# Kernel tuning notes

Hardware: AMD Instinct MI355X
Metric: run time of the kernel (lower is better)

The kernel has to match this reference:

```python
import jax, jax.numpy as jnp
import numpy as np

BN_EPS = 1e-6


def _conv1x1(x, w, b):
    # x: (B, Cin, N, K), w: (Cout, Cin), b: (Cout,)
    return jnp.einsum('oc,bcnk->bonk', w, x) + b[None, :, None, None]


def _bn(x, gamma, beta, mean, var):
    # inference-mode BatchNorm2d over channel axis 1
    inv = gamma / jnp.sqrt(var + BN_EPS)
    return x * inv[None, :, None, None] + (beta - mean * inv)[None, :, None, None]


def setup_inputs() -> dict:
    key = jax.random.key(0)
    ks = jax.random.split(key, 12)
    B, N, K = 4, 16384, 16
    C_out = 32
    C_img = 2 * C_out - 10          # 54, so concat has 2*C_out = 64 channels
    C_in1 = 2 * C_out               # 64
    C_in2 = 2 * (C_out + 3)         # 70

    points = jax.random.normal(ks[0], (B, N, 3), jnp.float32)
    image_features = jax.random.normal(ks[1], (B, C_img, N, K), jnp.float32)
    dist = jax.random.uniform(ks[2], (B, N, K), jnp.float32)
    idx = jax.random.randint(ks[3], (B, N, K), 0, N, dtype=jnp.int32)

    w1 = jax.random.normal(ks[4], (C_out, C_in1), jnp.float32) / np.sqrt(C_in1).astype(np.float32)
    b1 = jnp.zeros((C_out,), jnp.float32)
    gamma1 = jnp.ones((C_out,), jnp.float32)
    beta1 = jnp.zeros((C_out,), jnp.float32)
    mean1 = 0.1 * jax.random.normal(ks[5], (C_out,), jnp.float32)
    var1 = 0.5 + jax.random.uniform(ks[6], (C_out,), jnp.float32)

    w2 = jax.random.normal(ks[7], (C_out, C_in2), jnp.float32) / np.sqrt(C_in2).astype(np.float32)
    b2 = jnp.zeros((C_out,), jnp.float32)
    gamma2 = jnp.ones((C_out,), jnp.float32)
    beta2 = jnp.zeros((C_out,), jnp.float32)
    mean2 = 0.1 * jax.random.normal(ks[8], (C_out,), jnp.float32)
    var2 = 0.5 + jax.random.uniform(ks[9], (C_out,), jnp.float32)

    return {
        'points': points, 'image_features': image_features, 'dist': dist, 'idx': idx,
        'w1': w1, 'b1': b1, 'gamma1': gamma1, 'beta1': beta1, 'mean1': mean1, 'var1': var1,
        'w2': w2, 'b2': b2, 'gamma2': gamma2, 'beta2': beta2, 'mean2': mean2, 'var2': var2,
    }


def reference(points, image_features, dist, idx,
              w1, b1, gamma1, beta1, mean1, var1,
              w2, b2, gamma2, beta2, mean2, var2):
    B, N, K = idx.shape
    pts = jnp.swapaxes(points, 1, 2)                       # (B, 3, N)
    ep = jnp.broadcast_to(pts[:, :, :, None], (B, 3, N, K))  # extended points
    # KNN gather: nb[b, c, n, k] = pts[b, c, idx[b, n, k]]
    nb = jax.vmap(lambda p, i: p[:, i])(pts, idx)          # (B, 3, N, K)

    concat = jnp.concatenate(
        [ep, nb, ep - nb, dist[:, None, :, :], image_features], axis=1)  # (B, 64, N, K)

    h = jax.nn.relu(_bn(_conv1x1(concat, w1, b1), gamma1, beta1, mean1, var1))  # (B, 32, N, K)
    feat = jnp.concatenate([h, ep], axis=1)                # (B, 35, N, K)

    pooled = jnp.concatenate(
        [jnp.max(feat, axis=-1, keepdims=True),
         jnp.mean(feat, axis=-1, keepdims=True)], axis=1)  # (B, 70, N, 1)

    out = jax.nn.relu(_bn(_conv1x1(pooled, w2, b2), gamma2, beta2, mean2, var2))  # (B, 32, N, 1)
    return out
```

## Files before the change

kernel.cpp:

```cpp
#include <hip/hip_runtime.h>
#include <hip/hip_bf16.h>
#include <cmath>

#define BN_EPS 1e-6f
typedef unsigned int u32;
typedef __attribute__((ext_vector_type(8))) short short8;
typedef __attribute__((ext_vector_type(4))) float f32x4;

constexpr int B_    = 4;
constexpr int N_    = 16384;
constexpr int K_    = 16;
constexpr int C_IMG = 54;
constexpr int C1    = 64;
constexpr int CO    = 32;
constexpr int C2    = 70;
constexpr int NT    = 16;
constexpr int POS   = 256;
constexpr int XSTR  = 34;
constexpr int PPAD  = 76;
constexpr int NK    = N_ * K_;
constexpr int CHUNK = 6;

__device__ inline u32 pkbf(float a, float b) {
    union { __hip_bfloat162 h; u32 u; } cv;
    cv.h = __float22bfloat162_rn(make_float2(a, b));
    return cv.u;
}

__global__ __launch_bounds__(256, 4) void pif_mfma_kernel(
    const float* __restrict__ points, const float* __restrict__ imgf,
    const float* __restrict__ dist,   const int*   __restrict__ idx,
    const float* __restrict__ w1, const float* __restrict__ b1,
    const float* __restrict__ g1, const float* __restrict__ be1,
    const float* __restrict__ m1, const float* __restrict__ v1,
    const float* __restrict__ w2, const float* __restrict__ b2,
    const float* __restrict__ g2, const float* __restrict__ be2,
    const float* __restrict__ m2, const float* __restrict__ v2,
    float* __restrict__ out)
{
    __shared__ u32   x_lds[POS * XSTR];
    __shared__ float pooled[NT][PPAD];

    const int t   = threadIdx.x;
    const int tpb = N_ / NT;
    const int b   = blockIdx.x / tpb;
    const int n0  = (blockIdx.x % tpb) * NT;
    const int k   = t & 15, ln = t >> 4, n = n0 + ln;

    const int   base_nk = (b * N_ + n) * K_ + k;
    const int   j  = idx[base_nk];
    const float dv = dist[base_nk];
    const int   pb = (b * N_ + n) * 3;
    const float px = points[pb], py = points[pb + 1], pz = points[pb + 2];
    const int   qb = (b * N_ + j) * 3;
    const float qx = points[qb], qy = points[qb + 1], qz = points[qb + 2];

    u32* row = &x_lds[t * XSTR];
    row[0] = pkbf(px, py);
    row[1] = pkbf(pz, qx);
    row[2] = pkbf(qy, qz);
    row[3] = pkbf(px - qx, py - qy);
    row[4] = pkbf(pz - qz, dv);

    const float* ip = imgf + (size_t)b * C_IMG * NK + (n * K_ + k);
    #pragma unroll
    for (int c0 = 0; c0 < C_IMG; c0 += CHUNK) {
        float xv[CHUNK];
        #pragma unroll
        for (int jj = 0; jj < CHUNK; ++jj) xv[jj] = ip[(c0 + jj) * NK];
        row[5 + c0 / 2    ] = pkbf(xv[0], xv[1]);
        row[5 + c0 / 2 + 1] = pkbf(xv[2], xv[3]);
        row[5 + c0 / 2 + 2] = pkbf(xv[4], xv[5]);
    }

    const int w = t >> 6, lane = t & 63, m16 = lane & 15, quad = lane >> 4;

    short8 bfrag[2][2];
    float  inv1v[2], add1v[2];
    #pragma unroll
    for (int ot = 0; ot < 2; ++ot) {
        const int o = ot * 16 + m16;
        #pragma unroll
        for (int kc = 0; kc < 2; ++kc) {
            const float* wr = w1 + o * C1 + kc * 32 + quad * 8;
            union { u32 u[4]; short8 v; } bf;
            bf.u[0] = pkbf(wr[0], wr[1]); bf.u[1] = pkbf(wr[2], wr[3]);
            bf.u[2] = pkbf(wr[4], wr[5]); bf.u[3] = pkbf(wr[6], wr[7]);
            bfrag[ot][kc] = bf.v;
        }
        const float iv = g1[o] * rsqrtf(v1[o] + BN_EPS);
        inv1v[ot] = iv;
        add1v[ot] = be1[o] - m1[o] * iv + b1[o] * iv;
    }

    if (t < 48) {
        const int nn = t & 15, jj = t >> 4;
        const float v = points[(b * N_ + n0 + nn) * 3 + jj];
        pooled[nn][32 + jj] = v;
        pooled[nn][67 + jj] = v;
    }

    __syncthreads();

    f32x4 acc[4][2];
    #pragma unroll
    for (int mt = 0; mt < 4; ++mt)
        #pragma unroll
        for (int ot = 0; ot < 2; ++ot)
            acc[mt][ot] = (f32x4){0.f, 0.f, 0.f, 0.f};

    #pragma unroll
    for (int mt = 0; mt < 4; ++mt) {
        #pragma unroll
        for (int kc = 0; kc < 2; ++kc) {
            const u32* r2 = &x_lds[(w * 64 + mt * 16 + m16) * XSTR + kc * 16 + quad * 4];
            uint2 a0 = *(const uint2*)r2;
            uint2 a1 = *(const uint2*)(r2 + 2);
            union { u32 u[4]; short8 v; } af;
            af.u[0] = a0.x; af.u[1] = a0.y; af.u[2] = a1.x; af.u[3] = a1.y;
            acc[mt][0] = __builtin_amdgcn_mfma_f32_16x16x32_bf16(af.v, bfrag[0][kc], acc[mt][0], 0, 0, 0);
            acc[mt][1] = __builtin_amdgcn_mfma_f32_16x16x32_bf16(af.v, bfrag[1][kc], acc[mt][1], 0, 0, 0);
        }
    }

    #pragma unroll
    for (int mt = 0; mt < 4; ++mt) {
        #pragma unroll
        for (int ot = 0; ot < 2; ++ot) {
            float mx = 0.f, sm = 0.f;
            #pragma unroll
            for (int r = 0; r < 4; ++r) {
                float hv = fmaf(acc[mt][ot][r], inv1v[ot], add1v[ot]);
                hv = fmaxf(hv, 0.f);
                mx = fmaxf(mx, hv);
                sm += hv;
            }
            mx = fmaxf(mx, __shfl_xor(mx, 16));
            mx = fmaxf(mx, __shfl_xor(mx, 32));
            sm += __shfl_xor(sm, 16);
            sm += __shfl_xor(sm, 32);
            if (quad == 0) {
                const int nn = w * 4 + mt;
                pooled[nn][ot * 16 + m16]      = mx;
                pooled[nn][35 + ot * 16 + m16] = sm * (1.f / 16.f);
            }
        }
    }
    __syncthreads();

    #pragma unroll
    for (int r = 0; r < 2; ++r) {
        const int nn = t & 15;
        const int o  = (t >> 4) + r * 16;
        const float* wr = w2 + o * C2;
        float a0 = 0.f, a1 = 0.f;
        #pragma unroll
        for (int c = 0; c < C2; c += 2) {
            a0 = fmaf(wr[c],     pooled[nn][c],     a0);
            a1 = fmaf(wr[c + 1], pooled[nn][c + 1], a1);
        }
        const float acc2 = a0 + a1;
        const float iv = g2[o] * rsqrtf(v2[o] + BN_EPS);
        float ov = fmaf(acc2 + b2[o], iv, be2[o] - m2[o] * iv);
        ov = fmaxf(ov, 0.f);
        out[(b * CO + o) * N_ + n0 + nn] = ov;
    }
}

extern "C" void kernel_launch(void* const* d_in, const int* in_sizes, int n_in,
                              void* d_out, int out_size, void* d_ws, size_t ws_size,
                              hipStream_t stream) {
    const float* points = (const float*)d_in[0];
    const float* imgf   = (const float*)d_in[1];
    const float* dist   = (const float*)d_in[2];
    const int*   idx    = (const int*)  d_in[3];
    const float* w1     = (const float*)d_in[4];
    const float* b1     = (const float*)d_in[5];
    const float* g1     = (const float*)d_in[6];
    const float* be1    = (const float*)d_in[7];
    const float* m1     = (const float*)d_in[8];
    const float* v1     = (const float*)d_in[9];
    const float* w2     = (const float*)d_in[10];
    const float* b2     = (const float*)d_in[11];
    const float* g2     = (const float*)d_in[12];
    const float* be2    = (const float*)d_in[13];
    const float* m2     = (const float*)d_in[14];
    const float* v2     = (const float*)d_in[15];
    float* out          = (float*)d_out;

    const int blocks = B_ * (N_ / NT);
    pif_mfma_kernel<<<blocks, 256, 0, stream>>>(
        points, imgf, dist, idx,
        w1, b1, g1, be1, m1, v1,
        w2, b2, g2, be2, m2, v2, out);
}
```

Measured before the change: 356.9 us.

## Vectorize image-feature loads with float4 and transpose LDS staging to channel-major

```diff
diff --git a/kernel.cpp b/kernel.cpp
--- a/kernel.cpp
+++ b/kernel.cpp
@@ -16,10 +16,12 @@
 constexpr int C2    = 70;
 constexpr int NT    = 16;
 constexpr int POS   = 256;
-constexpr int XSTR  = 34;
+constexpr int XT    = 260;
 constexpr int PPAD  = 76;
 constexpr int NK    = N_ * K_;
-constexpr int CHUNK = 6;
+constexpr int NCP   = C_IMG / 2;
+constexpr int ITEMS = NCP * (POS / 4);
+constexpr int ITERS = (ITEMS + 255) / 256;
 
 __device__ inline u32 pkbf(float a, float b) {
     union { __hip_bfloat162 h; u32 u; } cv;
@@ -38,15 +40,28 @@
     const float* __restrict__ m2, const float* __restrict__ v2,
     float* __restrict__ out)
 {
-    __shared__ u32   x_lds[POS * XSTR];
+    __shared__ u32   x_lds[32 * XT];
     __shared__ float pooled[NT][PPAD];
 
     const int t   = threadIdx.x;
     const int tpb = N_ / NT;
     const int b   = blockIdx.x / tpb;
     const int n0  = (blockIdx.x % tpb) * NT;
-    const int k   = t & 15, ln = t >> 4, n = n0 + ln;
-
+
+    const float* ib = imgf + (size_t)b * C_IMG * NK + n0 * K_;
+    float4 va[ITERS], vb[ITERS];
+    #pragma unroll
+    for (int jj = 0; jj < ITERS; ++jj) {
+        if (jj < ITERS - 1 || t < ITEMS - (ITERS - 1) * 256) {
+            const int item = t + jj * 256;
+            const int cp = item >> 6, q = item & 63;
+            const float* p0 = ib + (size_t)(2 * cp) * NK + 4 * q;
+            va[jj] = *(const float4*)p0;
+            vb[jj] = *(const float4*)(p0 + NK);
+        }
+    }
+
+    const int k = t & 15, ln = t >> 4, n = n0 + ln;
     const int   base_nk = (b * N_ + n) * K_ + k;
     const int   j  = idx[base_nk];
     const float dv = dist[base_nk];
@@ -55,22 +70,24 @@
     const int   qb = (b * N_ + j) * 3;
     const float qx = points[qb], qy = points[qb + 1], qz = points[qb + 2];
 
-    u32* row = &x_lds[t * XSTR];
-    row[0] = pkbf(px, py);
-    row[1] = pkbf(pz, qx);
-    row[2] = pkbf(qy, qz);
-    row[3] = pkbf(px - qx, py - qy);
-    row[4] = pkbf(pz - qz, dv);
-
-    const float* ip = imgf + (size_t)b * C_IMG * NK + (n * K_ + k);
-    #pragma unroll
-    for (int c0 = 0; c0 < C_IMG; c0 += CHUNK) {
-        float xv[CHUNK];
-        #pragma unroll
-        for (int jj = 0; jj < CHUNK; ++jj) xv[jj] = ip[(c0 + jj) * NK];
-        row[5 + c0 / 2    ] = pkbf(xv[0], xv[1]);
-        row[5 + c0 / 2 + 1] = pkbf(xv[2], xv[3]);
-        row[5 + c0 / 2 + 2] = pkbf(xv[4], xv[5]);
+    x_lds[0 * XT + t] = pkbf(px, py);
+    x_lds[1 * XT + t] = pkbf(pz, qx);
+    x_lds[2 * XT + t] = pkbf(qy, qz);
+    x_lds[3 * XT + t] = pkbf(px - qx, py - qy);
+    x_lds[4 * XT + t] = pkbf(pz - qz, dv);
+
+    #pragma unroll
+    for (int jj = 0; jj < ITERS; ++jj) {
+        if (jj < ITERS - 1 || t < ITEMS - (ITERS - 1) * 256) {
+            const int item = t + jj * 256;
+            const int cp = item >> 6, q = item & 63;
+            uint4 pk;
+            pk.x = pkbf(va[jj].x, vb[jj].x);
+            pk.y = pkbf(va[jj].y, vb[jj].y);
+            pk.z = pkbf(va[jj].z, vb[jj].z);
+            pk.w = pkbf(va[jj].w, vb[jj].w);
+            *(uint4*)&x_lds[(5 + cp) * XT + 4 * q] = pk;
+        }
     }
 
     const int w = t >> 6, lane = t & 63, m16 = lane & 15, quad = lane >> 4;
@@ -111,13 +128,15 @@
 
     #pragma unroll
     for (int mt = 0; mt < 4; ++mt) {
+        const int prow = w * 64 + mt * 16 + m16;
         #pragma unroll
         for (int kc = 0; kc < 2; ++kc) {
-            const u32* r2 = &x_lds[(w * 64 + mt * 16 + m16) * XSTR + kc * 16 + quad * 4];
-            uint2 a0 = *(const uint2*)r2;
-            uint2 a1 = *(const uint2*)(r2 + 2);
+            const u32* cb = &x_lds[(kc * 16 + quad * 4) * XT + prow];
             union { u32 u[4]; short8 v; } af;
-            af.u[0] = a0.x; af.u[1] = a0.y; af.u[2] = a1.x; af.u[3] = a1.y;
+            af.u[0] = cb[0];
+            af.u[1] = cb[XT];
+            af.u[2] = cb[2 * XT];
+            af.u[3] = cb[3 * XT];
             acc[mt][0] = __builtin_amdgcn_mfma_f32_16x16x32_bf16(af.v, bfrag[0][kc], acc[mt][0], 0, 0, 0);
             acc[mt][1] = __builtin_amdgcn_mfma_f32_16x16x32_bf16(af.v, bfrag[1][kc], acc[mt][1], 0, 0, 0);
         }
```

After: 359.2 us. Within noise of the previous version (+0.6%).

## Stream image features directly into LDS via global_load_lds in channel-major fp32 layout

Applied to the files above, without the earlier changes.

```diff
diff --git a/kernel.cpp b/kernel.cpp
--- a/kernel.cpp
+++ b/kernel.cpp
@@ -16,10 +16,9 @@
 constexpr int C2    = 70;
 constexpr int NT    = 16;
 constexpr int POS   = 256;
-constexpr int XSTR  = 34;
+constexpr int XT    = 256;
 constexpr int PPAD  = 76;
 constexpr int NK    = N_ * K_;
-constexpr int CHUNK = 6;
 
 __device__ inline u32 pkbf(float a, float b) {
     union { __hip_bfloat162 h; u32 u; } cv;
@@ -27,7 +26,7 @@
     return cv.u;
 }
 
-__global__ __launch_bounds__(256, 4) void pif_mfma_kernel(
+__global__ __launch_bounds__(256, 2) void pif_mfma_kernel(
     const float* __restrict__ points, const float* __restrict__ imgf,
     const float* __restrict__ dist,   const int*   __restrict__ idx,
     const float* __restrict__ w1, const float* __restrict__ b1,
@@ -38,42 +37,51 @@
     const float* __restrict__ m2, const float* __restrict__ v2,
     float* __restrict__ out)
 {
-    __shared__ u32   x_lds[POS * XSTR];
+    __shared__ float xf[64 * XT];
     __shared__ float pooled[NT][PPAD];
 
-    const int t   = threadIdx.x;
-    const int tpb = N_ / NT;
-    const int b   = blockIdx.x / tpb;
-    const int n0  = (blockIdx.x % tpb) * NT;
-    const int k   = t & 15, ln = t >> 4, n = n0 + ln;
-
+    const int t    = threadIdx.x;
+    const int tpb  = N_ / NT;
+    const int b    = blockIdx.x / tpb;
+    const int n0   = (blockIdx.x % tpb) * NT;
+    const int lane = t & 63;
+    const int w    = t >> 6;
+
+    const int k = t & 15, ln = t >> 4, n = n0 + ln;
     const int   base_nk = (b * N_ + n) * K_ + k;
     const int   j  = idx[base_nk];
     const float dv = dist[base_nk];
+
+    const float* ib = imgf + (size_t)b * C_IMG * NK + n0 * K_;
+    #pragma unroll
+    for (int i = 0; i < 14; ++i) {
+        const int c = w + 4 * i;
+        if (c < C_IMG) {
+            const float* gsrc = ib + (size_t)c * NK + (lane << 2);
+            float* ldst = &xf[(10 + c) * XT];
+            __builtin_amdgcn_global_load_lds(
+                (const __attribute__((address_space(1))) void*)gsrc,
+                (__attribute__((address_space(3))) void*)ldst, 16, 0, 0);
+        }
+    }
+
     const int   pb = (b * N_ + n) * 3;
     const float px = points[pb], py = points[pb + 1], pz = points[pb + 2];
     const int   qb = (b * N_ + j) * 3;
     const float qx = points[qb], qy = points[qb + 1], qz = points[qb + 2];
 
-    u32* row = &x_lds[t * XSTR];
-    row[0] = pkbf(px, py);
-    row[1] = pkbf(pz, qx);
-    row[2] = pkbf(qy, qz);
-    row[3] = pkbf(px - qx, py - qy);
-    row[4] = pkbf(pz - qz, dv);
-
-    const float* ip = imgf + (size_t)b * C_IMG * NK + (n * K_ + k);
-    #pragma unroll
-    for (int c0 = 0; c0 < C_IMG; c0 += CHUNK) {
-        float xv[CHUNK];
-        #pragma unroll
-        for (int jj = 0; jj < CHUNK; ++jj) xv[jj] = ip[(c0 + jj) * NK];
-        row[5 + c0 / 2    ] = pkbf(xv[0], xv[1]);
-        row[5 + c0 / 2 + 1] = pkbf(xv[2], xv[3]);
-        row[5 + c0 / 2 + 2] = pkbf(xv[4], xv[5]);
-    }
-
-    const int w = t >> 6, lane = t & 63, m16 = lane & 15, quad = lane >> 4;
+    xf[0 * XT + t] = px;
+    xf[1 * XT + t] = py;
+    xf[2 * XT + t] = pz;
+    xf[3 * XT + t] = qx;
+    xf[4 * XT + t] = qy;
+    xf[5 * XT + t] = qz;
+    xf[6 * XT + t] = px - qx;
+    xf[7 * XT + t] = py - qy;
+    xf[8 * XT + t] = pz - qz;
+    xf[9 * XT + t] = dv;
+
+    const int m16 = lane & 15, quad = lane >> 4;
 
     short8 bfrag[2][2];
     float  inv1v[2], add1v[2];
@@ -111,13 +119,17 @@
 
     #pragma unroll
     for (int mt = 0; mt < 4; ++mt) {
+        const int prow = w * 64 + mt * 16 + m16;
         #pragma unroll
         for (int kc = 0; kc < 2; ++kc) {
-            const u32* r2 = &x_lds[(w * 64 + mt * 16 + m16) * XSTR + kc * 16 + quad * 4];
-            uint2 a0 = *(const uint2*)r2;
-            uint2 a1 = *(const uint2*)(r2 + 2);
+            const float* cb = &xf[(kc * 32 + quad * 8) * XT + prow];
+            float v0 = cb[0 * XT], v1_ = cb[1 * XT], v2_ = cb[2 * XT], v3 = cb[3 * XT];
+            float v4 = cb[4 * XT], v5 = cb[5 * XT], v6 = cb[6 * XT], v7 = cb[7 * XT];
             union { u32 u[4]; short8 v; } af;
-            af.u[0] = a0.x; af.u[1] = a0.y; af.u[2] = a1.x; af.u[3] = a1.y;
+            af.u[0] = pkbf(v0, v1_);
+            af.u[1] = pkbf(v2_, v3);
+            af.u[2] = pkbf(v4, v5);
+            af.u[3] = pkbf(v6, v7);
             acc[mt][0] = __builtin_amdgcn_mfma_f32_16x16x32_bf16(af.v, bfrag[0][kc], acc[mt][0], 0, 0, 0);
             acc[mt][1] = __builtin_amdgcn_mfma_f32_16x16x32_bf16(af.v, bfrag[1][kc], acc[mt][1], 0, 0, 0);
         }
```

Result: no change. 356.0 us (-0.3%).

## Double-buffer image features into LDS via async global_load_lds over multi-step blocks

Applied to the files above, without the earlier changes.

```diff
diff --git a/kernel.cpp b/kernel.cpp
--- a/kernel.cpp
+++ b/kernel.cpp
@@ -14,12 +14,17 @@
 constexpr int C1    = 64;
 constexpr int CO    = 32;
 constexpr int C2    = 70;
-constexpr int NT    = 16;
-constexpr int POS   = 256;
-constexpr int XSTR  = 34;
-constexpr int PPAD  = 76;
 constexpr int NK    = N_ * K_;
-constexpr int CHUNK = 6;
+
+constexpr int NTB   = 64;
+constexpr int NSTEP = 8;
+constexpr int SN    = 8;
+constexpr int SPOS  = 128;
+constexpr int BPOS  = 1024;
+constexpr int IST   = 260;
+constexpr int CST   = 1028;
+constexpr int TPB   = N_ / NTB;
+constexpr int NBLK  = B_ * TPB;
 
 __device__ inline u32 pkbf(float a, float b) {
     union { __hip_bfloat162 h; u32 u; } cv;
@@ -27,7 +32,13 @@
     return cv.u;
 }
 
-__global__ __launch_bounds__(256, 4) void pif_mfma_kernel(
+__device__ inline void dma16(const float* gsrc, float* ldst) {
+    __builtin_amdgcn_global_load_lds(
+        (const __attribute__((address_space(1))) void*)gsrc,
+        (__attribute__((address_space(3))) void*)ldst, 16, 0, 0);
+}
+
+__global__ __launch_bounds__(256, 2) void pif_mfma_kernel(
     const float* __restrict__ points, const float* __restrict__ imgf,
     const float* __restrict__ dist,   const int*   __restrict__ idx,
     const float* __restrict__ w1, const float* __restrict__ b1,
@@ -38,42 +49,52 @@
     const float* __restrict__ m2, const float* __restrict__ v2,
     float* __restrict__ out)
 {
-    __shared__ u32   x_lds[POS * XSTR];
-    __shared__ float pooled[NT][PPAD];
-
-    const int t   = threadIdx.x;
-    const int tpb = N_ / NT;
-    const int b   = blockIdx.x / tpb;
-    const int n0  = (blockIdx.x % tpb) * NT;
-    const int k   = t & 15, ln = t >> 4, n = n0 + ln;
-
-    const int   base_nk = (b * N_ + n) * K_ + k;
-    const int   j  = idx[base_nk];
-    const float dv = dist[base_nk];
-    const int   pb = (b * N_ + n) * 3;
-    const float px = points[pb], py = points[pb + 1], pz = points[pb + 2];
-    const int   qb = (b * N_ + j) * 3;
-    const float qx = points[qb], qy = points[qb + 1], qz = points[qb + 2];
-
-    u32* row = &x_lds[t * XSTR];
-    row[0] = pkbf(px, py);
-    row[1] = pkbf(pz, qx);
-    row[2] = pkbf(qy, qz);
-    row[3] = pkbf(px - qx, py - qy);
-    row[4] = pkbf(pz - qz, dv);
-
-    const float* ip = imgf + (size_t)b * C_IMG * NK + (n * K_ + k);
+    __shared__ float imgf_lds[2][27][IST];
+    __shared__ u32   comp_lds[5][CST];
+    __shared__ float pooled[SN][77];
+
+    const int t = threadIdx.x;
+
+    const int g   = blockIdx.x;
+    const int sw  = (g & 7) * (NBLK / 8) + (g >> 3);
+    const int b   = sw / TPB;
+    const int bn0 = (sw % TPB) * NTB;
+
+    const int lane = t & 63, w = t >> 6;
+    const int m16 = lane & 15, quad = lane >> 4;
+
+    const int cp0 = (w < 3) ? w * 7 : 21;
+    const int ncp = (w < 3) ? 7 : 6;
+    const float* ib = imgf + (size_t)b * C_IMG * NK;
+    const int laneHi = lane >> 5, lane31 = lane & 31;
+
+    {
+        const int off0 = bn0 * K_;
+        for (int i = 0; i < ncp; ++i) {
+            const int cp = cp0 + i;
+            const float* gs = ib + (size_t)(2 * cp + laneHi) * NK + off0 + lane31 * 4;
+            dma16(gs, &imgf_lds[0][cp][0]);
+        }
+    }
+
     #pragma unroll
-    for (int c0 = 0; c0 < C_IMG; c0 += CHUNK) {
-        float xv[CHUNK];
-        #pragma unroll
-        for (int jj = 0; jj < CHUNK; ++jj) xv[jj] = ip[(c0 + jj) * NK];
-        row[5 + c0 / 2    ] = pkbf(xv[0], xv[1]);
-        row[5 + c0 / 2 + 1] = pkbf(xv[2], xv[3]);
-        row[5 + c0 / 2 + 2] = pkbf(xv[4], xv[5]);
-    }
-
-    const int w = t >> 6, lane = t & 63, m16 = lane & 15, quad = lane >> 4;
+    for (int c2 = 0; c2 < 4; ++c2) {
+        const int pos = c2 * 256 + t;
+        const int nl = pos >> 4, kk = pos & 15;
+        const int gn = bn0 + nl;
+        const int ii = (b * N_ + gn) * K_ + kk;
+        const int jx = idx[ii];
+        const float dvv = dist[ii];
+        const int pbo = (b * N_ + gn) * 3;
+        const float px = points[pbo], py = points[pbo + 1], pz = points[pbo + 2];
+        const int qbo = (b * N_ + jx) * 3;
+        const float qx = points[qbo], qy = points[qbo + 1], qz = points[qbo + 2];
+        comp_lds[0][pos] = pkbf(px, py);
+        comp_lds[1][pos] = pkbf(pz, qx);
+        comp_lds[2][pos] = pkbf(qy, qz);
+        comp_lds[3][pos] = pkbf(px - qx, py - qy);
+        comp_lds[4][pos] = pkbf(pz - qz, dvv);
+    }
 
     short8 bfrag[2][2];
     float  inv1v[2], add1v[2];
@@ -82,10 +103,14 @@
         const int o = ot * 16 + m16;
         #pragma unroll
         for (int kc = 0; kc < 2; ++kc) {
-            const float* wr = w1 + o * C1 + kc * 32 + quad * 8;
             union { u32 u[4]; short8 v; } bf;
-            bf.u[0] = pkbf(wr[0], wr[1]); bf.u[1] = pkbf(wr[2], wr[3]);
-            bf.u[2] = pkbf(wr[4], wr[5]); bf.u[3] = pkbf(wr[6], wr[7]);
+            #pragma unroll
+            for (int i2 = 0; i2 < 4; ++i2) {
+                const int lc0 = kc * 32 + quad * 8 + 2 * i2, lc1 = lc0 + 1;
+                const int c0 = (lc0 < 54) ? (10 + lc0) : (lc0 - 54);
+                const int c1 = (lc1 < 54) ? (10 + lc1) : (lc1 - 54);
+                bf.u[i2] = pkbf(w1[o * C1 + c0], w1[o * C1 + c1]);
+            }
             bfrag[ot][kc] = bf.v;
         }
         const float iv = g1[o] * rsqrtf(v1[o] + BN_EPS);
@@ -93,77 +118,124 @@
         add1v[ot] = be1[o] - m1[o] * iv + b1[o] * iv;
     }
 
-    if (t < 48) {
-        const int nn = t & 15, jj = t >> 4;
-        const float v = points[(b * N_ + n0 + nn) * 3 + jj];
-        pooled[nn][32 + jj] = v;
-        pooled[nn][67 + jj] = v;
-    }
+    const int nnC = t & 7, oC = t >> 3;
+    const float iv2 = g2[oC] * rsqrtf(v2[oC] + BN_EPS);
+    const float ad2 = be2[oC] - m2[oC] * iv2;
+    const float bb2 = b2[oC];
+    const float* wr2 = w2 + oC * C2;
 
     __syncthreads();
 
-    f32x4 acc[4][2];
-    #pragma unroll
-    for (int mt = 0; mt < 4; ++mt)
+    #pragma unroll 1
+    for (int s = 0; s < NSTEP; ++s) {
+        const int bb = s & 1;
+
+        if (s + 1 < NSTEP) {
+            const int offn = (bn0 + (s + 1) * SN) * K_;
+            for (int i = 0; i < ncp; ++i) {
+                const int cp = cp0 + i;
+                const float* gs = ib + (size_t)(2 * cp + laneHi) * NK + offn + lane31 * 4;
+                dma16(gs, &imgf_lds[bb ^ 1][cp][0]);
+            }
+            if (w < 3) asm volatile("s_waitcnt vmcnt(7)" ::: "memory");
+            else       asm volatile("s_waitcnt vmcnt(6)" ::: "memory");
+        } else {
+            asm volatile("s_waitcnt vmcnt(0)" ::: "memory");
+        }
+        __builtin_amdgcn_s_barrier();
+        __builtin_amdgcn_sched_barrier(0);
+
+        if (t < 24) {
+            const int jj = t >> 3, nn2 = t & 7;
+            const float v = points[(b * N_ + bn0 + s * SN + nn2) * 3 + jj];
+            pooled[nn2][32 + jj] = v;
+            pooled[nn2][67 + jj] = v;
+        }
+
+        const float* Xi = &imgf_lds[bb][0][0];
+        const int pco = s * SPOS;
+
         #pragma unroll
-        for (int ot = 0; ot < 2; ++ot)
-            acc[mt][ot] = (f32x4){0.f, 0.f, 0.f, 0.f};
-
-    #pragma unroll
-    for (int mt = 0; mt < 4; ++mt) {
-        #pragma unroll
-        for (int kc = 0; kc < 2; ++kc) {
-            const u32* r2 = &x_lds[(w * 64 + mt * 16 + m16) * XSTR + kc * 16 + quad * 4];
-            uint2 a0 = *(const uint2*)r2;
-            uint2 a1 = *(const uint2*)(r2 + 2);
-            union { u32 u[4]; short8 v; } af;
-            af.u[0] = a0.x; af.u[1] = a0.y; af.u[2] = a1.x; af.u[3] = a1.y;
-            acc[mt][0] = __builtin_amdgcn_mfma_f32_16x16x32_bf16(af.v, bfrag[0][kc], acc[mt][0], 0, 0, 0);
-            acc[mt][1] = __builtin_amdgcn_mfma_f32_16x16x32_bf16(af.v, bfrag[1][kc], acc[mt][1], 0, 0, 0);
-        }
-    }
-
-    #pragma unroll
-    for (int mt = 0; mt < 4; ++mt) {
-        #pragma unroll
-        for (int ot = 0; ot < 2; ++ot) {
-            float mx = 0.f, sm = 0.f;
-            #pragma unroll
-            for (int r = 0; r < 4; ++r) {
-                float hv = fmaf(acc[mt][ot][r], inv1v[ot], add1v[ot]);
-                hv = fmaxf(hv, 0.f);
-                mx = fmaxf(mx, hv);
-                sm += hv;
-            }
-            mx = fmaxf(mx, __shfl_xor(mx, 16));
-            mx = fmaxf(mx, __shfl_xor(mx, 32));
-            sm += __shfl_xor(sm, 16);
-            sm += __shfl_xor(sm, 32);
-            if (quad == 0) {
-                const int nn = w * 4 + mt;
-                pooled[nn][ot * 16 + m16]      = mx;
-                pooled[nn][35 + ot * 16 + m16] = sm * (1.f / 16.f);
-            }
-        }
-    }
-    __syncthreads();
-
-    #pragma unroll
-    for (int r = 0; r < 2; ++r) {
-        const int nn = t & 15;
-        const int o  = (t >> 4) + r * 16;
-        const float* wr = w2 + o * C2;
-        float a0 = 0.f, a1 = 0.f;
-        #pragma unroll
-        for (int c = 0; c < C2; c += 2) {
-            a0 = fmaf(wr[c],     pooled[nn][c],     a0);
-            a1 = fmaf(wr[c + 1], pooled[nn][c + 1], a1);
-        }
-        const float acc2 = a0 + a1;
-        const float iv = g2[o] * rsqrtf(v2[o] + BN_EPS);
-        float ov = fmaf(acc2 + b2[o], iv, be2[o] - m2[o] * iv);
-        ov = fmaxf(ov, 0.f);
-        out[(b * CO + o) * N_ + n0 + nn] = ov;
+        for (int u = 0; u < 2; ++u) {
+            const int m = 2 * w + u;
+            const int p = m * 16 + m16;
+            f32x4 acc0 = (f32x4){0.f, 0.f, 0.f, 0.f};
+            f32x4 acc1 = (f32x4){0.f, 0.f, 0.f, 0.f};
+
+            #pragma unroll
+            for (int kc = 0; kc < 2; ++kc) {
+                union { u32 uu[4]; short8 v; } af;
+                if (kc == 0) {
+                    #pragma unroll
+                    for (int i2 = 0; i2 < 4; ++i2) {
+                        const float* cb = Xi + (quad * 4 + i2) * IST + p;
+                        af.uu[i2] = pkbf(cb[0], cb[128]);
+                    }
+                } else {
+                    if (quad < 2) {
+                        #pragma unroll
+                        for (int i2 = 0; i2 < 4; ++i2) {
+                            const float* cb = Xi + (16 + quad * 4 + i2) * IST + p;
+                            af.uu[i2] = pkbf(cb[0], cb[128]);
+                        }
+                    } else if (quad == 2) {
+                        #pragma unroll
+                        for (int i2 = 0; i2 < 3; ++i2) {
+                            const float* cb = Xi + (24 + i2) * IST + p;
+                            af.uu[i2] = pkbf(cb[0], cb[128]);
+                        }
+                        af.uu[3] = comp_lds[0][pco + p];
+                    } else {
+                        #pragma unroll
+                        for (int i2 = 0; i2 < 4; ++i2)
+                            af.uu[i2] = comp_lds[1 + i2][pco + p];
+                    }
+                }
+                acc0 = __builtin_amdgcn_mfma_f32_16x16x32_bf16(af.v, bfrag[0][kc], acc0, 0, 0, 0);
+                acc1 = __builtin_amdgcn_mfma_f32_16x16x32_bf16(af.v, bfrag[1][kc], acc1, 0, 0, 0);
+            }
+
+            #pragma unroll
+            for (int ot = 0; ot < 2; ++ot) {
+                const f32x4 aa = ot ? acc1 : acc0;
+                float mx = 0.f, sm = 0.f;
+                #pragma unroll
+                for (int r = 0; r < 4; ++r) {
+                    float hv = fmaf(aa[r], inv1v[ot], add1v[ot]);
+                    hv = fmaxf(hv, 0.f);
+                    mx = fmaxf(mx, hv);
+                    sm += hv;
+                }
+                mx = fmaxf(mx, __shfl_xor(mx, 16));
+                mx = fmaxf(mx, __shfl_xor(mx, 32));
+                sm += __shfl_xor(sm, 16);
+                sm += __shfl_xor(sm, 32);
+                if (quad == 0) {
+                    pooled[m][ot * 16 + m16]      = mx;
+                    pooled[m][35 + ot * 16 + m16] = sm * (1.f / 16.f);
+                }
+            }
+        }
+
+        asm volatile("s_waitcnt lgkmcnt(0)" ::: "memory");
+        __builtin_amdgcn_s_barrier();
+        __builtin_amdgcn_sched_barrier(0);
+
+        {
+            float a0 = 0.f, a1 = 0.f;
+            #pragma unroll
+            for (int c = 0; c < C2; c += 2) {
+                a0 = fmaf(wr2[c],     pooled[nnC][c],     a0);
+                a1 = fmaf(wr2[c + 1], pooled[nnC][c + 1], a1);
+            }
+            float ov = fmaf((a0 + a1) + bb2, iv2, ad2);
+            ov = fmaxf(ov, 0.f);
+            out[(b * CO + oC) * N_ + bn0 + s * SN + nnC] = ov;
+        }
+
+        asm volatile("s_waitcnt lgkmcnt(0)" ::: "memory");
+        __builtin_amdgcn_s_barrier();
+        __builtin_amdgcn_sched_barrier(0);
     }
 }
 
@@ -188,8 +260,7 @@
     const float* v2     = (const float*)d_in[15];
     float* out          = (float*)d_out;
 
-    const int blocks = B_ * (N_ / NT);
-    pif_mfma_kernel<<<blocks, 256, 0, stream>>>(
+    pif_mfma_kernel<<<NBLK, 256, 0, stream>>>(
         points, imgf, dist, idx,
         w1, b1, g1, be1, m1, v1,
         w2, b2, g2, be2, m2, v2, out);
```

Result: no change. 362.2 us (+1.5%).
